# Kernel tuning notes

Measured on AMD Instinct MI355X. Metric: run time of the kernel, lower is better.

## Reference

```python
import jax, jax.numpy as jnp
import numpy as np

# ---- module hyperparameters (from init_kwargs) ----
R, C = 16, 16            # layer.rows, layer.cols
STRIDE = 0               # layer.stride (shared receptive field)
KH = KW = 8              # layer.kernel_size
CIN, COUT = 16, 64       # in/out channels
T = 7                    # spike time steps (== maxweight)
MAXW = 7.0
UCAPTURE, UMINUS, USEARCH, UBACKOFF, UMIN = 0.102, 0.051, 0.032, 0.96, 0.008


def setup_inputs() -> dict:
    key = jax.random.key(0)
    k1, k2, k3 = jax.random.split(key, 3)
    input_spikes = jax.random.randint(k1, (T, CIN, KH, KW), 0, 2).astype(jnp.int32)
    output_spikes = jax.random.randint(k2, (T, COUT, R, C), 0, 2).astype(jnp.int32)
    # integer-valued weights in [0, maxweight], stored as float for the update math
    weight = jax.random.randint(k3, (R, C, COUT, CIN, KH, KW), 0, int(MAXW) + 1).astype(jnp.float32)
    return {"weight": weight, "input_spikes": input_spikes, "output_spikes": output_spikes}


def reference(weight, input_spikes, output_spikes):
    # spike-time codes: fewer spikes -> later time
    x_times = int(MAXW) - jnp.sum(input_spikes, axis=0)    # [CIN, KH, KW] (H==KH, W==KW)
    y_times = int(MAXW) - jnp.sum(output_spikes, axis=0)   # [COUT, R, C]

    # gather the receptive-field patch for every (row, col) column (static indices)
    rr = (np.arange(R) * STRIDE)[:, None] + np.arange(KH)  # [R, KH]
    cc = (np.arange(C) * STRIDE)[:, None] + np.arange(KW)  # [C, KW]
    # advanced indexing -> [CIN, R, C, KH, KW]
    x_patch = x_times[:, rr[:, None, :, None], cc[None, :, None, :]]
    bx = jnp.transpose(x_patch, (1, 2, 0, 3, 4))[:, :, None, :, :, :]   # [R,C,1,CIN,KH,KW]
    by = jnp.transpose(y_times, (1, 2, 0))[:, :, :, None, None, None]   # [R,C,COUT,1,1,1]

    A = bx == int(MAXW)
    B = by == int(MAXW)
    Cgt = bx > by

    zero = jnp.float32(0.0)
    probs_plus = jnp.where(~A & B, USEARCH, jnp.where(~A & ~B & ~Cgt, UCAPTURE, zero))
    probs_minus = jnp.where(A & ~B, UBACKOFF, jnp.where(~A & ~B & Cgt, UMINUS, zero))
    # broadcast to full weight shape
    shape = weight.shape
    probs_plus = jnp.broadcast_to(probs_plus, shape)
    probs_minus = jnp.broadcast_to(probs_minus, shape)

    key = jax.random.key(42)
    k1, k2, k3, k4, k5 = jax.random.split(key, 5)
    dt = weight.dtype
    bern_plus = (jax.random.uniform(k1, shape) < probs_plus)
    bern_minus = (jax.random.uniform(k2, shape) < probs_minus)

    ratio = weight * (1.0 / MAXW)
    F_minus_raw = jax.random.uniform(k3, shape) < (1.0 - ratio) * (1.0 + ratio)
    F_plus_raw = jax.random.uniform(k4, shape) < ratio * (2.0 - ratio)
    umin_bern = jax.random.uniform(k5, shape) < UMIN
    # torch.max of two {0,1} frames == logical OR
    F_plus = jnp.logical_or(F_plus_raw, umin_bern).astype(dt)
    F_minus = jnp.logical_or(F_minus_raw, umin_bern).astype(dt)

    new_w = weight + bern_plus.astype(dt) * F_plus - bern_minus.astype(dt) * F_minus
    new_w = jnp.clip(new_w, 0.0, MAXW)  # integer-valued floats, cast to int in torch
    return new_w
```

## Files before the change

### kernel.cpp

```cpp
#include <hip/hip_runtime.h>
#include <stdint.h>


#define N_TOTAL 16777216
#define Y_SIZE 16384
#define X_SIZE 1024

struct U2 { uint32_t a, b; };

constexpr uint32_t rotl_c(uint32_t x, int r) {
  return (x << r) | (x >> (32 - r));
}

constexpr U2 threefry_c(uint32_t k0, uint32_t k1, uint32_t x0, uint32_t x1) {
  uint32_t ks2 = k0 ^ k1 ^ 0x1BD11BDAu;
  x0 += k0; x1 += k1;
  x0 += x1; x1 = rotl_c(x1, 13); x1 ^= x0;
  x0 += x1; x1 = rotl_c(x1, 15); x1 ^= x0;
  x0 += x1; x1 = rotl_c(x1, 26); x1 ^= x0;
  x0 += x1; x1 = rotl_c(x1, 6);  x1 ^= x0;
  x0 += k1; x1 += ks2 + 1u;
  x0 += x1; x1 = rotl_c(x1, 17); x1 ^= x0;
  x0 += x1; x1 = rotl_c(x1, 29); x1 ^= x0;
  x0 += x1; x1 = rotl_c(x1, 16); x1 ^= x0;
  x0 += x1; x1 = rotl_c(x1, 24); x1 ^= x0;
  x0 += ks2; x1 += k0 + 2u;
  x0 += x1; x1 = rotl_c(x1, 13); x1 ^= x0;
  x0 += x1; x1 = rotl_c(x1, 15); x1 ^= x0;
  x0 += x1; x1 = rotl_c(x1, 26); x1 ^= x0;
  x0 += x1; x1 = rotl_c(x1, 6);  x1 ^= x0;
  x0 += k0; x1 += k1 + 3u;
  x0 += x1; x1 = rotl_c(x1, 17); x1 ^= x0;
  x0 += x1; x1 = rotl_c(x1, 29); x1 ^= x0;
  x0 += x1; x1 = rotl_c(x1, 16); x1 ^= x0;
  x0 += x1; x1 = rotl_c(x1, 24); x1 ^= x0;
  x0 += k1; x1 += ks2 + 4u;
  x0 += x1; x1 = rotl_c(x1, 13); x1 ^= x0;
  x0 += x1; x1 = rotl_c(x1, 15); x1 ^= x0;
  x0 += x1; x1 = rotl_c(x1, 26); x1 ^= x0;
  x0 += x1; x1 = rotl_c(x1, 6);  x1 ^= x0;
  x0 += ks2; x1 += k0 + 5u;
  return {x0, x1};
}

constexpr U2 SK1 = threefry_c(0u, 42u, 0u, 0u);
constexpr U2 SK2 = threefry_c(0u, 42u, 0u, 1u);
constexpr U2 SK3 = threefry_c(0u, 42u, 0u, 2u);
constexpr U2 SK4 = threefry_c(0u, 42u, 0u, 3u);
constexpr U2 SK5 = threefry_c(0u, 42u, 0u, 4u);

constexpr uint32_t KS2_1 = SK1.a ^ SK1.b ^ 0x1BD11BDAu;
constexpr uint32_t KS2_2 = SK2.a ^ SK2.b ^ 0x1BD11BDAu;
constexpr uint32_t KS2_3 = SK3.a ^ SK3.b ^ 0x1BD11BDAu;
constexpr uint32_t KS2_4 = SK4.a ^ SK4.b ^ 0x1BD11BDAu;
constexpr uint32_t KS2_5 = SK5.a ^ SK5.b ^ 0x1BD11BDAu;

constexpr uint32_t bern_thr(float pf) {
  double p8 = (double)pf * 8388608.0;
  uint64_t t = (uint64_t)p8;
  if ((double)t < p8) t += 1u;
  return (uint32_t)(t << 9);
}
constexpr uint32_t T_SEARCH  = bern_thr(0.032f);
constexpr uint32_t T_CAPTURE = bern_thr(0.102f);
constexpr uint32_t T_BACKOFF = bern_thr(0.96f);
constexpr uint32_t T_MINUS   = bern_thr(0.051f);
constexpr uint32_t T_UMIN    = bern_thr(0.008f);

__device__ __forceinline__ uint32_t rotl_d(uint32_t x, int r) {
  return __builtin_amdgcn_alignbit(x, x, 32 - r);
}

__device__ __forceinline__ uint32_t tf_fold_k(uint32_t k0, uint32_t k1,
                                              uint32_t ks2, uint32_t ctr) {
  uint32_t x0 = k0;
  uint32_t x1 = ctr + k1;
  x0 += x1; x1 = rotl_d(x1, 13); x1 ^= x0;
  x0 += x1; x1 = rotl_d(x1, 15); x1 ^= x0;
  x0 += x1; x1 = rotl_d(x1, 26); x1 ^= x0;
  x0 += x1; x1 = rotl_d(x1, 6);  x1 ^= x0;
  x0 += k1; x1 += ks2 + 1u;
  x0 += x1; x1 = rotl_d(x1, 17); x1 ^= x0;
  x0 += x1; x1 = rotl_d(x1, 29); x1 ^= x0;
  x0 += x1; x1 = rotl_d(x1, 16); x1 ^= x0;
  x0 += x1; x1 = rotl_d(x1, 24); x1 ^= x0;
  x0 += ks2; x1 += k0 + 2u;
  x0 += x1; x1 = rotl_d(x1, 13); x1 ^= x0;
  x0 += x1; x1 = rotl_d(x1, 15); x1 ^= x0;
  x0 += x1; x1 = rotl_d(x1, 26); x1 ^= x0;
  x0 += x1; x1 = rotl_d(x1, 6);  x1 ^= x0;
  x0 += k0; x1 += k1 + 3u;
  x0 += x1; x1 = rotl_d(x1, 17); x1 ^= x0;
  x0 += x1; x1 = rotl_d(x1, 29); x1 ^= x0;
  x0 += x1; x1 = rotl_d(x1, 16); x1 ^= x0;
  x0 += x1; x1 = rotl_d(x1, 24); x1 ^= x0;
  x0 += k1; x1 += ks2 + 4u;
  x0 += x1; x1 = rotl_d(x1, 13); x1 ^= x0;
  x0 += x1; x1 = rotl_d(x1, 15); x1 ^= x0;
  x0 += x1; x1 = rotl_d(x1, 26); x1 ^= x0;
  x0 += x1; x1 = rotl_d(x1, 6);  x1 ^= x0;
  x0 += ks2; x1 += k0 + 5u;
  return x0 ^ x1;
}

__device__ __forceinline__ float bits_to_unit_float(uint32_t bits) {
  uint32_t fb = (bits >> 9) | 0x3f800000u;
  return __uint_as_float(fb) - 1.0f;
}

__device__ __forceinline__ uint32_t mbcnt64(uint64_t m) {
  return __builtin_amdgcn_mbcnt_hi((uint32_t)(m >> 32),
         __builtin_amdgcn_mbcnt_lo((uint32_t)m, 0u));
}

__device__ __forceinline__ bool helper_ok(uint2 rc) {
  bool sm = (rc.x >> 31) != 0u;
  uint32_t ctr = rc.x & 0x7fffffffu;
  float wf = __uint_as_float(rc.y);
  const float inv7 = (float)(1.0 / 7.0);
  float ratio = __fmul_rn(wf, inv7);
  float thrF = sm
      ? __fmul_rn(__fsub_rn(1.0f, ratio), __fadd_rn(1.0f, ratio))
      : __fmul_rn(ratio, __fsub_rn(2.0f, ratio));
  uint32_t k0 = sm ? SK3.a : SK4.a;
  uint32_t k1 = sm ? SK3.b : SK4.b;
  uint32_t ks = sm ? KS2_3 : KS2_4;
  uint32_t b34 = tf_fold_k(k0, k1, ks, ctr);
  uint32_t b5 = tf_fold_k(SK5.a, SK5.b, KS2_5, ctr);
  return (bits_to_unit_float(b34) < thrF) | (b5 < T_UMIN);
}

__global__ void precompute_times(const int* __restrict__ in_sp,
                                 const int* __restrict__ out_sp,
                                 int* __restrict__ xt, int* __restrict__ yt) {
  int tid = blockIdx.x * 256 + threadIdx.x;
  if (tid < Y_SIZE) {
    int s = 0;
#pragma unroll
    for (int t = 0; t < 7; ++t) s += out_sp[t * Y_SIZE + tid];
    yt[tid] = 7 - s;
  } else if (tid < Y_SIZE + X_SIZE) {
    int j = tid - Y_SIZE;
    int s = 0;
#pragma unroll
    for (int t = 0; t < 7; ++t) s += in_sp[t * X_SIZE + j];
    xt[j] = 7 - s;
  }
}

__global__ __launch_bounds__(256) void modstdp8(const float* __restrict__ w,
                                                const int* __restrict__ xt,
                                                const int* __restrict__ yt,
                                                float* __restrict__ out) {
  __shared__ uint2 rec[4 * 512];
  __shared__ uint64_t okm[4 * 8];

  uint32_t tid = threadIdx.x;
  uint32_t lane = tid & 63u;
  uint32_t ws = tid >> 6;
  uint32_t t = blockIdx.x * 256u + tid;
  uint32_t i0 = t * 8u;

  float4 wa = *reinterpret_cast<const float4*>(w + i0);
  float4 wb = *reinterpret_cast<const float4*>(w + i0 + 4u);
  int4 xa = *reinterpret_cast<const int4*>(xt + (i0 & 1023u));
  int4 xb = *reinterpret_cast<const int4*>(xt + (i0 & 1023u) + 4u);
  float warr[8];
  *reinterpret_cast<float4*>(warr) = wa;
  *reinterpret_cast<float4*>(warr + 4) = wb;
  int barr[8];
  *reinterpret_cast<int4*>(barr) = xa;
  *reinterpret_cast<int4*>(barr + 4) = xb;

  uint32_t cout = (i0 >> 10) & 63u;
  uint32_t c = (i0 >> 16) & 15u;
  uint32_t r = i0 >> 20;
  int by = yt[cout * 256u + r * 16u + c];
  bool B = (by == 7);
  int mb6 = min(by, 6);

  bool hit[8], sM[8];
  uint32_t rank[8];
  uint32_t cnt = 0;

#pragma unroll
  for (int e = 0; e < 8; ++e) {
    uint32_t i = i0 + (uint32_t)e;
    int bx = barr[e];
    bool A = (bx == 7);
    bool selm = (!B) && (bx > mb6);
    sM[e] = selm;
    uint32_t thr = selm ? (A ? T_BACKOFF : T_MINUS)
                        : (B ? (A ? 0u : T_SEARCH) : T_CAPTURE);
    uint32_t k0 = selm ? SK2.a : SK1.a;
    uint32_t k1 = selm ? SK2.b : SK1.b;
    uint32_t ks = selm ? KS2_2 : KS2_1;
    uint32_t bits12 = tf_fold_k(k0, k1, ks, i);
    bool h = bits12 < thr;
    hit[e] = h;

    uint64_t m = __ballot(h);
    uint32_t rk = 0;
    if (h) {
      rk = cnt + mbcnt64(m);
      rec[ws * 512u + rk] = make_uint2(i | (selm ? 0x80000000u : 0u),
                                       __float_as_uint(warr[e]));
    }
    rank[e] = rk;
    cnt += (uint32_t)__popcll(m);
  }

  uint64_t okmask0;
  {
    bool ok = false;
    if (lane < cnt) ok = helper_ok(rec[ws * 512u + lane]);
    okmask0 = __ballot(ok);
  }

  if (__builtin_expect(cnt > 64u, 0)) {
    if (lane == 0u) okm[ws * 8u] = okmask0;
    for (uint32_t base = 64u; base < cnt; base += 64u) {
      bool ok = false;
      uint32_t idx = base + lane;
      if (idx < cnt) ok = helper_ok(rec[ws * 512u + idx]);
      uint64_t mm = __ballot(ok);
      if (lane == 0u) okm[ws * 8u + (base >> 6)] = mm;
    }
    float res[8];
#pragma unroll
    for (int e = 0; e < 8; ++e) {
      uint64_t mask = okm[ws * 8u + (rank[e] >> 6)];
      uint32_t ob = (uint32_t)(mask >> (rank[e] & 63u)) & 1u;
      float d = (hit[e] && ob) ? (sM[e] ? -1.0f : 1.0f) : 0.0f;
      res[e] = __builtin_amdgcn_fmed3f(warr[e] + d, 0.0f, 7.0f);
    }
    *reinterpret_cast<float4*>(out + i0) = *reinterpret_cast<float4*>(res);
    *reinterpret_cast<float4*>(out + i0 + 4u) =
        *reinterpret_cast<float4*>(res + 4);
  } else {
    float res[8];
#pragma unroll
    for (int e = 0; e < 8; ++e) {
      uint32_t ob = (uint32_t)(okmask0 >> rank[e]) & 1u;
      float d = (hit[e] && ob) ? (sM[e] ? -1.0f : 1.0f) : 0.0f;
      res[e] = __builtin_amdgcn_fmed3f(warr[e] + d, 0.0f, 7.0f);
    }
    *reinterpret_cast<float4*>(out + i0) = *reinterpret_cast<float4*>(res);
    *reinterpret_cast<float4*>(out + i0 + 4u) =
        *reinterpret_cast<float4*>(res + 4);
  }
}

extern "C" void kernel_launch(void* const* d_in, const int* in_sizes, int n_in,
                              void* d_out, int out_size, void* d_ws, size_t ws_size,
                              hipStream_t stream) {
  const float* w = (const float*)d_in[0];
  const int* isp = (const int*)d_in[1];
  const int* osp = (const int*)d_in[2];
  float* out = (float*)d_out;
  int* xt = (int*)d_ws;
  int* yt = ((int*)d_ws) + X_SIZE;

  precompute_times<<<(Y_SIZE + X_SIZE + 255) / 256, 256, 0, stream>>>(isp, osp, xt, yt);
  modstdp8<<<N_TOTAL / 8 / 256, 256, 0, stream>>>(w, xt, yt, out);
}
```

Baseline: 59.10 us.

## Pack hit records into 32 bits and scatter accepted updates directly to output

```diff
diff --git a/kernel.cpp b/kernel.cpp
--- a/kernel.cpp
+++ b/kernel.cpp
@@ -113,23 +113,6 @@
          __builtin_amdgcn_mbcnt_lo((uint32_t)m, 0u));
 }
 
-__device__ __forceinline__ bool helper_ok(uint2 rc) {
-  bool sm = (rc.x >> 31) != 0u;
-  uint32_t ctr = rc.x & 0x7fffffffu;
-  float wf = __uint_as_float(rc.y);
-  const float inv7 = (float)(1.0 / 7.0);
-  float ratio = __fmul_rn(wf, inv7);
-  float thrF = sm
-      ? __fmul_rn(__fsub_rn(1.0f, ratio), __fadd_rn(1.0f, ratio))
-      : __fmul_rn(ratio, __fsub_rn(2.0f, ratio));
-  uint32_t k0 = sm ? SK3.a : SK4.a;
-  uint32_t k1 = sm ? SK3.b : SK4.b;
-  uint32_t ks = sm ? KS2_3 : KS2_4;
-  uint32_t b34 = tf_fold_k(k0, k1, ks, ctr);
-  uint32_t b5 = tf_fold_k(SK5.a, SK5.b, KS2_5, ctr);
-  return (bits_to_unit_float(b34) < thrF) | (b5 < T_UMIN);
-}
-
 __global__ void precompute_times(const int* __restrict__ in_sp,
                                  const int* __restrict__ out_sp,
                                  int* __restrict__ xt, int* __restrict__ yt) {
@@ -148,12 +131,11 @@
   }
 }
 
-__global__ __launch_bounds__(256) void modstdp8(const float* __restrict__ w,
-                                                const int* __restrict__ xt,
-                                                const int* __restrict__ yt,
-                                                float* __restrict__ out) {
-  __shared__ uint2 rec[4 * 512];
-  __shared__ uint64_t okm[4 * 8];
+__global__ __launch_bounds__(256) void modstdp8s(const float* __restrict__ w,
+                                                 const int* __restrict__ xt,
+                                                 const int* __restrict__ yt,
+                                                 float* __restrict__ out) {
+  __shared__ uint32_t rec[4 * 512];
 
   uint32_t tid = threadIdx.x;
   uint32_t lane = tid & 63u;
@@ -177,10 +159,10 @@
   uint32_t r = i0 >> 20;
   int by = yt[cout * 256u + r * 16u + c];
   bool B = (by == 7);
-  int mb6 = min(by, 6);
-
-  bool hit[8], sM[8];
-  uint32_t rank[8];
+  int gate = B ? 8 : min(by, 6);
+  uint32_t tNS_A = B ? 0u : T_CAPTURE;
+  uint32_t tNS_nA = B ? T_SEARCH : T_CAPTURE;
+
   uint32_t cnt = 0;
 
 #pragma unroll
@@ -188,66 +170,56 @@
     uint32_t i = i0 + (uint32_t)e;
     int bx = barr[e];
     bool A = (bx == 7);
-    bool selm = (!B) && (bx > mb6);
-    sM[e] = selm;
-    uint32_t thr = selm ? (A ? T_BACKOFF : T_MINUS)
-                        : (B ? (A ? 0u : T_SEARCH) : T_CAPTURE);
+    bool selm = bx > gate;
+    uint32_t tS = A ? T_BACKOFF : T_MINUS;
+    uint32_t tN = A ? tNS_A : tNS_nA;
+    uint32_t thr = selm ? tS : tN;
     uint32_t k0 = selm ? SK2.a : SK1.a;
     uint32_t k1 = selm ? SK2.b : SK1.b;
     uint32_t ks = selm ? KS2_2 : KS2_1;
     uint32_t bits12 = tf_fold_k(k0, k1, ks, i);
     bool h = bits12 < thr;
-    hit[e] = h;
 
     uint64_t m = __ballot(h);
-    uint32_t rk = 0;
     if (h) {
-      rk = cnt + mbcnt64(m);
-      rec[ws * 512u + rk] = make_uint2(i | (selm ? 0x80000000u : 0u),
-                                       __float_as_uint(warr[e]));
+      uint32_t rk = cnt + mbcnt64(m);
+      uint32_t wi = (uint32_t)warr[e];
+      rec[ws * 512u + rk] = i | (wi << 24) | (selm ? 0x08000000u : 0u);
     }
-    rank[e] = rk;
     cnt += (uint32_t)__popcll(m);
   }
 
-  uint64_t okmask0;
-  {
-    bool ok = false;
-    if (lane < cnt) ok = helper_ok(rec[ws * 512u + lane]);
-    okmask0 = __ballot(ok);
-  }
-
-  if (__builtin_expect(cnt > 64u, 0)) {
-    if (lane == 0u) okm[ws * 8u] = okmask0;
-    for (uint32_t base = 64u; base < cnt; base += 64u) {
-      bool ok = false;
-      uint32_t idx = base + lane;
-      if (idx < cnt) ok = helper_ok(rec[ws * 512u + idx]);
-      uint64_t mm = __ballot(ok);
-      if (lane == 0u) okm[ws * 8u + (base >> 6)] = mm;
+  *reinterpret_cast<float4*>(out + i0) = wa;
+  *reinterpret_cast<float4*>(out + i0 + 4u) = wb;
+
+  asm volatile("s_waitcnt vmcnt(0)" ::: "memory");
+
+  for (uint32_t base = 0; base < cnt; base += 64u) {
+    uint32_t idx = base + lane;
+    if (idx < cnt) {
+      uint32_t rc = rec[ws * 512u + idx];
+      uint32_t ctr = rc & 0x00FFFFFFu;
+      uint32_t wi = (rc >> 24) & 7u;
+      bool sm = (rc & 0x08000000u) != 0u;
+      float wf = (float)wi;
+
+      const float inv7 = (float)(1.0 / 7.0);
+      float ratio = __fmul_rn(wf, inv7);
+      float thrF = sm
+          ? __fmul_rn(__fsub_rn(1.0f, ratio), __fadd_rn(1.0f, ratio))
+          : __fmul_rn(ratio, __fsub_rn(2.0f, ratio));
+      uint32_t k0 = sm ? SK3.a : SK4.a;
+      uint32_t k1 = sm ? SK3.b : SK4.b;
+      uint32_t ks = sm ? KS2_3 : KS2_4;
+      uint32_t b34 = tf_fold_k(k0, k1, ks, ctr);
+      uint32_t b5 = tf_fold_k(SK5.a, SK5.b, KS2_5, ctr);
+      bool ok = (bits_to_unit_float(b34) < thrF) | (b5 < T_UMIN);
+      if (ok) {
+        int nw = sm ? (int)wi - 1 : (int)wi + 1;
+        nw = max(min(nw, 7), 0);
+        out[ctr] = (float)nw;
+      }
     }
-    float res[8];
-#pragma unroll
-    for (int e = 0; e < 8; ++e) {
-      uint64_t mask = okm[ws * 8u + (rank[e] >> 6)];
-      uint32_t ob = (uint32_t)(mask >> (rank[e] & 63u)) & 1u;
-      float d = (hit[e] && ob) ? (sM[e] ? -1.0f : 1.0f) : 0.0f;
-      res[e] = __builtin_amdgcn_fmed3f(warr[e] + d, 0.0f, 7.0f);
-    }
-    *reinterpret_cast<float4*>(out + i0) = *reinterpret_cast<float4*>(res);
-    *reinterpret_cast<float4*>(out + i0 + 4u) =
-        *reinterpret_cast<float4*>(res + 4);
-  } else {
-    float res[8];
-#pragma unroll
-    for (int e = 0; e < 8; ++e) {
-      uint32_t ob = (uint32_t)(okmask0 >> rank[e]) & 1u;
-      float d = (hit[e] && ob) ? (sM[e] ? -1.0f : 1.0f) : 0.0f;
-      res[e] = __builtin_amdgcn_fmed3f(warr[e] + d, 0.0f, 7.0f);
-    }
-    *reinterpret_cast<float4*>(out + i0) = *reinterpret_cast<float4*>(res);
-    *reinterpret_cast<float4*>(out + i0 + 4u) =
-        *reinterpret_cast<float4*>(res + 4);
   }
 }
 
@@ -262,5 +234,5 @@
   int* yt = ((int*)d_ws) + X_SIZE;
 
   precompute_times<<<(Y_SIZE + X_SIZE + 255) / 256, 256, 0, stream>>>(isp, osp, xt, yt);
-  modstdp8<<<N_TOTAL / 8 / 256, 256, 0, stream>>>(w, xt, yt, out);
-}
+  modstdp8s<<<N_TOTAL / 8 / 256, 256, 0, stream>>>(w, xt, yt, out);
+}
```

Measured after the change: 58.13 us. No clear change (-1.7%).
